# Optimization experiments

Measured on AMD Instinct MI355X. Metric: run time of the kernel, lower is better.

The kernel has to match this reference:

```python
import jax, jax.numpy as jnp
import numpy as np

B, C, H, W = 4, 384, 128, 128
HEADS = 8
EPS = 1e-12  # torch F.normalize default eps


def setup_inputs() -> dict:
    key = jax.random.key(0)
    k1, k2, k3, k4 = jax.random.split(key, 4)
    in1 = jax.random.normal(k1, (B, C, H, W), dtype=jnp.float32)
    in2 = jax.random.normal(k2, (B, C, H, W), dtype=jnp.float32)
    temperature = jnp.ones((HEADS, 1, 1), dtype=jnp.float32)
    proj_w = jax.random.normal(k3, (C, C), dtype=jnp.float32) * (1.0 / np.sqrt(C))
    proj_b = jax.random.normal(k4, (C,), dtype=jnp.float32) * 0.01
    return {"in1": in1, "in2": in2, "temperature": temperature,
            "proj_w": proj_w, "proj_b": proj_b}


def _l2norm_last(x):
    # torch F.normalize(dim=-1): x / max(||x||_2, eps)
    n = jnp.sqrt(jnp.sum(x * x, axis=-1, keepdims=True))
    return x / jnp.maximum(n, EPS)


def reference(in1, in2, temperature, proj_w, proj_b):
    b, c, h, w = in1.shape
    hd = c // HEADS  # per-head channels
    # b (head c) h w -> b head c (h w)
    q = in1.reshape(b, HEADS, hd, h * w)
    k = in2.reshape(b, HEADS, hd, h * w)
    q = _l2norm_last(q)
    k = _l2norm_last(k)
    # channel attention: [b, head, hd, hd]
    attn = jnp.einsum('bhcn,bhdn->bhcd', q, k) * temperature[None]
    attn = jax.nn.softmax(attn, axis=-1)
    out = jnp.einsum('bhcd,bhdn->bhcn', attn, k)  # [b, head, hd, HW]
    out = out.reshape(b, c, h, w)
    # 1x1 conv projection
    out = jnp.einsum('oc,bchw->bohw', proj_w, out) + proj_b[None, :, None, None]
    return out
```

## Files before the change

kernel.cpp:

```cpp
#include <hip/hip_runtime.h>
#include <hip/hip_bf16.h>

#define NB 4
#define CC 384
#define HEADS 8
#define HD 48
#define NN 16384
#define NROWS (NB*CC)

typedef __attribute__((ext_vector_type(8))) short bf16x8;
typedef __attribute__((ext_vector_type(4))) float f32x4;

__device__ __forceinline__ unsigned short f2bf(float f) {
  __hip_bfloat16 h = __float2bfloat16(f);
  return __builtin_bit_cast(unsigned short, h);
}
__device__ __forceinline__ unsigned int packbf(float a, float b) {
  return (unsigned int)f2bf(a) | ((unsigned int)f2bf(b) << 16);
}
__device__ __forceinline__ float bf2f(short s) {
  unsigned int u = ((unsigned int)(unsigned short)s) << 16;
  return __builtin_bit_cast(float, u);
}

__global__ __launch_bounds__(256) void k_copy(
    const float* __restrict__ in1, const float* __restrict__ in2,
    unsigned short* __restrict__ qbf, unsigned short* __restrict__ kbf)
{
  const float4* src = (const float4*)(blockIdx.y ? in2 : in1);
  uint4* dst = (uint4*)(blockIdx.y ? kbf : qbf);
  const int n = NROWS * NN / 8;
  int stride = gridDim.x * 256;
  for (int i = blockIdx.x * 256 + threadIdx.x; i < n; i += stride) {
    float4 v0 = src[2*i], v1 = src[2*i+1];
    uint4 o;
    o.x = packbf(v0.x, v0.y); o.y = packbf(v0.z, v0.w);
    o.z = packbf(v1.x, v1.y); o.w = packbf(v1.z, v1.w);
    dst[i] = o;
  }
}

__global__ __launch_bounds__(256) void k_gram(
    const unsigned short* __restrict__ qbf, const unsigned short* __restrict__ kbf,
    float* __restrict__ partial, float* __restrict__ sumsq_part)
{
  int bh = blockIdx.x;
  int chunk = blockIdx.y;
  int wave = threadIdx.x >> 6, lane = threadIdx.x & 63;
  int b = bh >> 3, h = bh & 7;
  size_t base = ((size_t)(b*CC + h*HD)) * NN;
  int lrow = lane & 15, lk = (lane >> 4) << 3;
  int kstart = chunk*1024 + wave*256;
  f32x4 acc[3][3] = {};
  float sq[3] = {0.f,0.f,0.f}, sk[3] = {0.f,0.f,0.f};
  for (int ks = 0; ks < 8; ++ks) {
    int kpos = kstart + ks*32 + lk;
    bf16x8 a[3], bb[3];
    #pragma unroll
    for (int t = 0; t < 3; ++t) {
      int rr = t*16 + lrow;
      a[t]  = *(const bf16x8*)(qbf + base + (size_t)rr * NN + kpos);
      bb[t] = *(const bf16x8*)(kbf + base + (size_t)rr * NN + kpos);
    }
    #pragma unroll
    for (int t = 0; t < 3; ++t) {
      #pragma unroll
      for (int j = 0; j < 8; ++j) {
        float fa = bf2f(a[t][j]);  sq[t] += fa*fa;
        float fb = bf2f(bb[t][j]); sk[t] += fb*fb;
      }
    }
    #pragma unroll
    for (int i = 0; i < 3; ++i)
      #pragma unroll
      for (int j = 0; j < 3; ++j)
        acc[i][j] = __builtin_amdgcn_mfma_f32_16x16x32_bf16(a[i], bb[j], acc[i][j], 0, 0, 0);
  }
  __shared__ float red[4][HD][HD+1];
  __shared__ float sqs[4][96];
  #pragma unroll
  for (int t = 0; t < 3; ++t) {
    float s = sq[t]; s += __shfl_xor(s, 16); s += __shfl_xor(s, 32);
    if (lane < 16) sqs[wave][t*16 + lane] = s;
    float s2 = sk[t]; s2 += __shfl_xor(s2, 16); s2 += __shfl_xor(s2, 32);
    if (lane < 16) sqs[wave][48 + t*16 + lane] = s2;
  }
  #pragma unroll
  for (int i = 0; i < 3; ++i)
    #pragma unroll
    for (int j = 0; j < 3; ++j)
      #pragma unroll
      for (int m = 0; m < 4; ++m) {
        int rr = i*16 + (lane>>4)*4 + m;
        int cc2 = j*16 + (lane&15);
        red[wave][rr][cc2] = acc[i][j][m];
      }
  __syncthreads();
  float* pout = partial + ((size_t)bh*16 + chunk) * (HD*HD);
  for (int e = threadIdx.x; e < HD*HD; e += 256) {
    int r = e / HD, c = e % HD;
    pout[e] = red[0][r][c] + red[1][r][c] + red[2][r][c] + red[3][r][c];
  }
  if (threadIdx.x < 96) {
    float* sout = sumsq_part + ((size_t)bh*16 + chunk) * 96;
    sout[threadIdx.x] = sqs[0][threadIdx.x] + sqs[1][threadIdx.x]
                      + sqs[2][threadIdx.x] + sqs[3][threadIdx.x];
  }
}

__global__ __launch_bounds__(256) void k_redsm(
    const float* __restrict__ partial, const float* __restrict__ sumsq_part,
    const float* __restrict__ temp, float* __restrict__ attn_out,
    float* __restrict__ rinv_k_g)
{
  int bh = blockIdx.x; int b = bh >> 3, h = bh & 7;
  __shared__ float attn[HD][HD+1];
  __shared__ float rqs[HD], rks[HD];
  if (threadIdx.x < 96) {
    float s = 0.f;
    #pragma unroll
    for (int c = 0; c < 16; ++c)
      s += sumsq_part[((size_t)bh*16 + c)*96 + threadIdx.x];
    float rinv = 1.f / fmaxf(sqrtf(s), 1e-12f);
    if (threadIdx.x < 48) rqs[threadIdx.x] = rinv;
    else { rks[threadIdx.x-48] = rinv; rinv_k_g[b*CC + h*HD + threadIdx.x-48] = rinv; }
  }
  const float* p = partial + (size_t)bh * 16 * (HD*HD);
  float tscale = temp[h];
  __syncthreads();
  for (int e = threadIdx.x; e < HD*HD; e += 256) {
    float s = 0.f;
    #pragma unroll
    for (int c2 = 0; c2 < 16; ++c2) s += p[c2*(HD*HD) + e];
    attn[e/HD][e%HD] = s * tscale * rqs[e/HD] * rks[e%HD];
  }
  __syncthreads();
  if (threadIdx.x < HD) {
    float* rowp = attn[threadIdx.x];
    float m = rowp[0];
    for (int j = 1; j < HD; ++j) m = fmaxf(m, rowp[j]);
    float sum = 0.f;
    for (int j = 0; j < HD; ++j) { float e = expf(rowp[j]-m); rowp[j] = e; sum += e; }
    float inv = 1.f / sum;
    for (int j = 0; j < HD; ++j) rowp[j] *= inv;
  }
  __syncthreads();
  float* ao = attn_out + (size_t)bh * (HD*HD);
  for (int e = threadIdx.x; e < HD*HD; e += 256)
    ao[e] = attn[e/HD][e%HD];
}

__global__ __launch_bounds__(256) void k_m(
    const float* __restrict__ attn, const float* __restrict__ proj_w,
    const float* __restrict__ rinv_k, unsigned short* __restrict__ Mbf)
{
  int b = blockIdx.x, ot = blockIdx.y;
  int o0 = ot * 16;
  __shared__ float sw[16*CC];
  __shared__ float sa[HEADS*HD*HD];
  const float* ab = attn + (size_t)b * HEADS * HD * HD;
  for (int i = threadIdx.x; i < HEADS*HD*HD; i += 256) sa[i] = ab[i];
  for (int i = threadIdx.x; i < 16*CC; i += 256)
    sw[i] = proj_w[(size_t)(o0 + i/CC)*CC + (i%CC)];
  __syncthreads();
  for (int idx = threadIdx.x; idx < 16*96; idx += 256) {
    int o = idx / 96, c4 = idx % 96;
    int col = c4 * 4;
    int h = col / HD, d = col % HD;
    const float* wp = sw + o*CC + h*HD;
    const float* ap = sa + h*HD*HD + d;
    f32x4 s = {0.f, 0.f, 0.f, 0.f};
    #pragma unroll
    for (int c2 = 0; c2 < HD; ++c2) {
      float w = wp[c2];
      f32x4 av = *(const f32x4*)(ap + c2*HD);
      s += w * av;
    }
    f32x4 rk = *(const f32x4*)(rinv_k + b*CC + col);
    s *= rk;
    ushort4 o4;
    o4.x = f2bf(s[0]); o4.y = f2bf(s[1]); o4.z = f2bf(s[2]); o4.w = f2bf(s[3]);
    *(ushort4*)(Mbf + ((size_t)b*CC + o0 + o)*CC + col) = o4;
  }
}

#define BM 128
#define BN 128
#define BK 64

__global__ __launch_bounds__(256) void k_final(
    const unsigned short* __restrict__ kbf, const unsigned short* __restrict__ Mbf,
    const float* __restrict__ bias, float* __restrict__ out)
{
  int b = blockIdx.z;
  int bm = blockIdx.y * BM, bn = blockIdx.x * BN;
  int tid = threadIdx.x, lane = tid & 63, wave = tid >> 6;
  int wrow = wave >> 1, wcol = wave & 1;
  __shared__ unsigned short Bt[BN * BK];
  char* btb = (char*)Bt;
  const unsigned short* kb = kbf + (size_t)b * CC * NN;
  const unsigned short* Mb = Mbf + (size_t)b * CC * CC;
  f32x4 acc[4][4] = {};
  int lrow = lane & 15, lkg = lane >> 4;
  for (int k0 = 0; k0 < CC; k0 += BK) {
    #pragma unroll
    for (int s = 0; s < 2; ++s) {
      int slot = tid + s*256;
      int cp = slot >> 4;
      int ng = slot & 15;
      int n0 = ng * 8;
      int c = k0 + cp*2;
      union { uint4 q; unsigned short u[8]; } r0, r1;
      r0.q = *(const uint4*)(kb + (size_t)c*NN + bn + n0);
      r1.q = *(const uint4*)(kb + (size_t)(c+1)*NN + bn + n0);
      #pragma unroll
      for (int i = 0; i < 8; ++i) {
        int n = n0 + i;
        unsigned int val = (unsigned int)r0.u[i] | ((unsigned int)r1.u[i] << 16);
        int pc = (cp>>2) ^ (n & 7) ^ ((n >> 3) & 7);
        *(unsigned int*)(btb + n*128 + (pc<<4) + ((cp&3)<<2)) = val;
      }
    }
    __syncthreads();
    #pragma unroll
    for (int kk = 0; kk < BK; kk += 32) {
      bf16x8 af[4], bfr[4];
      #pragma unroll
      for (int t = 0; t < 4; ++t) {
        int o = bm + wrow*64 + t*16 + lrow;
        af[t] = *(const bf16x8*)(Mb + (size_t)o*CC + (k0 + kk + (lkg<<3)));
        int n = wcol*64 + t*16 + lrow;
        int lc = (kk>>3) + lkg;
        int pc = lc ^ (n & 7) ^ ((n >> 3) & 7);
        bfr[t] = *(const bf16x8*)(btb + n*128 + (pc<<4));
      }
      #pragma unroll
      for (int i = 0; i < 4; ++i)
        #pragma unroll
        for (int j = 0; j < 4; ++j)
          acc[i][j] = __builtin_amdgcn_mfma_f32_16x16x32_bf16(af[i], bfr[j], acc[i][j], 0, 0, 0);
    }
    __syncthreads();
  }
  #pragma unroll
  for (int i = 0; i < 4; ++i) {
    int obase = bm + wrow*64 + i*16 + lkg*4;
    #pragma unroll
    for (int j = 0; j < 4; ++j) {
      int n = bn + wcol*64 + j*16 + lrow;
      #pragma unroll
      for (int m = 0; m < 4; ++m) {
        int o = obase + m;
        out[((size_t)b*CC + o)*NN + n] = acc[i][j][m] + bias[o];
      }
    }
  }
}

extern "C" void kernel_launch(void* const* d_in, const int* in_sizes, int n_in,
                              void* d_out, int out_size, void* d_ws, size_t ws_size,
                              hipStream_t stream)
{
  const float* in1    = (const float*)d_in[0];
  const float* in2    = (const float*)d_in[1];
  const float* temp   = (const float*)d_in[2];
  const float* proj_w = (const float*)d_in[3];
  const float* proj_b = (const float*)d_in[4];
  float* out = (float*)d_out;
  char* ws = (char*)d_ws;

  size_t off = 0;
  unsigned short* qbf = (unsigned short*)(ws + off); off += (size_t)NROWS*NN*2;
  unsigned short* kbf = (unsigned short*)(ws + off); off += (size_t)NROWS*NN*2;
  float* partial    = (float*)(ws + off); off += (size_t)32*16*HD*HD*4;
  float* sumsq_part = (float*)(ws + off); off += (size_t)32*16*96*4;
  float* attn_out   = (float*)(ws + off); off += (size_t)32*HD*HD*4;
  float* rinv_k     = (float*)(ws + off); off += NROWS*4;
  unsigned short* Mbf = (unsigned short*)(ws + off);

  k_copy<<<dim3(1024, 2), dim3(256), 0, stream>>>(in1, in2, qbf, kbf);
  k_gram<<<dim3(32, 16), dim3(256), 0, stream>>>(qbf, kbf, partial, sumsq_part);
  k_redsm<<<dim3(32), dim3(256), 0, stream>>>(partial, sumsq_part, temp, attn_out, rinv_k);
  k_m<<<dim3(NB, 24), dim3(256), 0, stream>>>(attn_out, proj_w, rinv_k, Mbf);
  k_final<<<dim3(NN/BN, CC/BM, NB), dim3(256), 0, stream>>>(kbf, Mbf, proj_b, out);
}
```

Before: 160.1 us.

## Fuse fp32-to-bf16 conversion into gram and final GEMM, drop copy kernel

Removes the standalone conversion kernel that wrote bf16 copies of both inputs. The gram kernel and the final projection GEMM now read the fp32 inputs directly and convert to bf16 in registers. The gram grid doubles its chunk count to keep parallelism, and sum-of-squares is now taken on fp32 values. This cuts a full write-then-read pass over the intermediate buffers, at the cost of the final GEMM loading twice the bytes per element of K.

```diff
diff --git a/kernel.cpp b/kernel.cpp
--- a/kernel.cpp
+++ b/kernel.cpp
@@ -18,30 +18,9 @@
 __device__ __forceinline__ unsigned int packbf(float a, float b) {
   return (unsigned int)f2bf(a) | ((unsigned int)f2bf(b) << 16);
 }
-__device__ __forceinline__ float bf2f(short s) {
-  unsigned int u = ((unsigned int)(unsigned short)s) << 16;
-  return __builtin_bit_cast(float, u);
-}
-
-__global__ __launch_bounds__(256) void k_copy(
+
+__global__ __launch_bounds__(256) void k_gram(
     const float* __restrict__ in1, const float* __restrict__ in2,
-    unsigned short* __restrict__ qbf, unsigned short* __restrict__ kbf)
-{
-  const float4* src = (const float4*)(blockIdx.y ? in2 : in1);
-  uint4* dst = (uint4*)(blockIdx.y ? kbf : qbf);
-  const int n = NROWS * NN / 8;
-  int stride = gridDim.x * 256;
-  for (int i = blockIdx.x * 256 + threadIdx.x; i < n; i += stride) {
-    float4 v0 = src[2*i], v1 = src[2*i+1];
-    uint4 o;
-    o.x = packbf(v0.x, v0.y); o.y = packbf(v0.z, v0.w);
-    o.z = packbf(v1.x, v1.y); o.w = packbf(v1.z, v1.w);
-    dst[i] = o;
-  }
-}
-
-__global__ __launch_bounds__(256) void k_gram(
-    const unsigned short* __restrict__ qbf, const unsigned short* __restrict__ kbf,
     float* __restrict__ partial, float* __restrict__ sumsq_part)
 {
   int bh = blockIdx.x;
@@ -50,25 +29,29 @@
   int b = bh >> 3, h = bh & 7;
   size_t base = ((size_t)(b*CC + h*HD)) * NN;
   int lrow = lane & 15, lk = (lane >> 4) << 3;
-  int kstart = chunk*1024 + wave*256;
+  int kstart = chunk*512 + wave*128;
   f32x4 acc[3][3] = {};
   float sq[3] = {0.f,0.f,0.f}, sk[3] = {0.f,0.f,0.f};
-  for (int ks = 0; ks < 8; ++ks) {
+  for (int ks = 0; ks < 4; ++ks) {
     int kpos = kstart + ks*32 + lk;
     bf16x8 a[3], bb[3];
     #pragma unroll
     for (int t = 0; t < 3; ++t) {
       int rr = t*16 + lrow;
-      a[t]  = *(const bf16x8*)(qbf + base + (size_t)rr * NN + kpos);
-      bb[t] = *(const bf16x8*)(kbf + base + (size_t)rr * NN + kpos);
-    }
-    #pragma unroll
-    for (int t = 0; t < 3; ++t) {
-      #pragma unroll
-      for (int j = 0; j < 8; ++j) {
-        float fa = bf2f(a[t][j]);  sq[t] += fa*fa;
-        float fb = bf2f(bb[t][j]); sk[t] += fb*fb;
-      }
+      const float* pq = in1 + base + (size_t)rr * NN + kpos;
+      const float* pk = in2 + base + (size_t)rr * NN + kpos;
+      float4 q0 = *(const float4*)pq, q1 = *((const float4*)pq + 1);
+      float4 k0 = *(const float4*)pk, k1 = *((const float4*)pk + 1);
+      union { bf16x8 v; unsigned short u[8]; } ua, ub;
+      ua.u[0]=f2bf(q0.x); ua.u[1]=f2bf(q0.y); ua.u[2]=f2bf(q0.z); ua.u[3]=f2bf(q0.w);
+      ua.u[4]=f2bf(q1.x); ua.u[5]=f2bf(q1.y); ua.u[6]=f2bf(q1.z); ua.u[7]=f2bf(q1.w);
+      ub.u[0]=f2bf(k0.x); ub.u[1]=f2bf(k0.y); ub.u[2]=f2bf(k0.z); ub.u[3]=f2bf(k0.w);
+      ub.u[4]=f2bf(k1.x); ub.u[5]=f2bf(k1.y); ub.u[6]=f2bf(k1.z); ub.u[7]=f2bf(k1.w);
+      a[t] = ua.v; bb[t] = ub.v;
+      sq[t] += q0.x*q0.x + q0.y*q0.y + q0.z*q0.z + q0.w*q0.w
+             + q1.x*q1.x + q1.y*q1.y + q1.z*q1.z + q1.w*q1.w;
+      sk[t] += k0.x*k0.x + k0.y*k0.y + k0.z*k0.z + k0.w*k0.w
+             + k1.x*k1.x + k1.y*k1.y + k1.z*k1.z + k1.w*k1.w;
     }
     #pragma unroll
     for (int i = 0; i < 3; ++i)
@@ -96,13 +79,13 @@
         red[wave][rr][cc2] = acc[i][j][m];
       }
   __syncthreads();
-  float* pout = partial + ((size_t)bh*16 + chunk) * (HD*HD);
+  float* pout = partial + ((size_t)bh*32 + chunk) * (HD*HD);
   for (int e = threadIdx.x; e < HD*HD; e += 256) {
     int r = e / HD, c = e % HD;
     pout[e] = red[0][r][c] + red[1][r][c] + red[2][r][c] + red[3][r][c];
   }
   if (threadIdx.x < 96) {
-    float* sout = sumsq_part + ((size_t)bh*16 + chunk) * 96;
+    float* sout = sumsq_part + ((size_t)bh*32 + chunk) * 96;
     sout[threadIdx.x] = sqs[0][threadIdx.x] + sqs[1][threadIdx.x]
                       + sqs[2][threadIdx.x] + sqs[3][threadIdx.x];
   }
@@ -119,19 +102,19 @@
   if (threadIdx.x < 96) {
     float s = 0.f;
     #pragma unroll
-    for (int c = 0; c < 16; ++c)
-      s += sumsq_part[((size_t)bh*16 + c)*96 + threadIdx.x];
+    for (int c = 0; c < 32; ++c)
+      s += sumsq_part[((size_t)bh*32 + c)*96 + threadIdx.x];
     float rinv = 1.f / fmaxf(sqrtf(s), 1e-12f);
     if (threadIdx.x < 48) rqs[threadIdx.x] = rinv;
     else { rks[threadIdx.x-48] = rinv; rinv_k_g[b*CC + h*HD + threadIdx.x-48] = rinv; }
   }
-  const float* p = partial + (size_t)bh * 16 * (HD*HD);
+  const float* p = partial + (size_t)bh * 32 * (HD*HD);
   float tscale = temp[h];
   __syncthreads();
   for (int e = threadIdx.x; e < HD*HD; e += 256) {
     float s = 0.f;
     #pragma unroll
-    for (int c2 = 0; c2 < 16; ++c2) s += p[c2*(HD*HD) + e];
+    for (int c2 = 0; c2 < 32; ++c2) s += p[c2*(HD*HD) + e];
     attn[e/HD][e%HD] = s * tscale * rqs[e/HD] * rks[e%HD];
   }
   __syncthreads();
@@ -189,7 +172,7 @@
 #define BK 64
 
 __global__ __launch_bounds__(256) void k_final(
-    const unsigned short* __restrict__ kbf, const unsigned short* __restrict__ Mbf,
+    const float* __restrict__ in2, const unsigned short* __restrict__ Mbf,
     const float* __restrict__ bias, float* __restrict__ out)
 {
   int b = blockIdx.z;
@@ -198,7 +181,7 @@
   int wrow = wave >> 1, wcol = wave & 1;
   __shared__ unsigned short Bt[BN * BK];
   char* btb = (char*)Bt;
-  const unsigned short* kb = kbf + (size_t)b * CC * NN;
+  const float* kb = in2 + (size_t)b * CC * NN;
   const unsigned short* Mb = Mbf + (size_t)b * CC * CC;
   f32x4 acc[4][4] = {};
   int lrow = lane & 15, lkg = lane >> 4;
@@ -210,13 +193,16 @@
       int ng = slot & 15;
       int n0 = ng * 8;
       int c = k0 + cp*2;
-      union { uint4 q; unsigned short u[8]; } r0, r1;
-      r0.q = *(const uint4*)(kb + (size_t)c*NN + bn + n0);
-      r1.q = *(const uint4*)(kb + (size_t)(c+1)*NN + bn + n0);
+      const float* p0 = kb + (size_t)c*NN + bn + n0;
+      const float* p1 = kb + (size_t)(c+1)*NN + bn + n0;
+      float4 a0 = *(const float4*)p0, a1 = *((const float4*)p0 + 1);
+      float4 b0 = *(const float4*)p1, b1 = *((const float4*)p1 + 1);
+      float lo[8] = {a0.x,a0.y,a0.z,a0.w,a1.x,a1.y,a1.z,a1.w};
+      float hi[8] = {b0.x,b0.y,b0.z,b0.w,b1.x,b1.y,b1.z,b1.w};
       #pragma unroll
       for (int i = 0; i < 8; ++i) {
         int n = n0 + i;
-        unsigned int val = (unsigned int)r0.u[i] | ((unsigned int)r1.u[i] << 16);
+        unsigned int val = packbf(lo[i], hi[i]);
         int pc = (cp>>2) ^ (n & 7) ^ ((n >> 3) & 7);
         *(unsigned int*)(btb + n*128 + (pc<<4) + ((cp&3)<<2)) = val;
       }
@@ -270,17 +256,14 @@
   char* ws = (char*)d_ws;
 
   size_t off = 0;
-  unsigned short* qbf = (unsigned short*)(ws + off); off += (size_t)NROWS*NN*2;
-  unsigned short* kbf = (unsigned short*)(ws + off); off += (size_t)NROWS*NN*2;
-  float* partial    = (float*)(ws + off); off += (size_t)32*16*HD*HD*4;
-  float* sumsq_part = (float*)(ws + off); off += (size_t)32*16*96*4;
+  float* partial    = (float*)(ws + off); off += (size_t)32*32*HD*HD*4;
+  float* sumsq_part = (float*)(ws + off); off += (size_t)32*32*96*4;
   float* attn_out   = (float*)(ws + off); off += (size_t)32*HD*HD*4;
   float* rinv_k     = (float*)(ws + off); off += NROWS*4;
   unsigned short* Mbf = (unsigned short*)(ws + off);
 
-  k_copy<<<dim3(1024, 2), dim3(256), 0, stream>>>(in1, in2, qbf, kbf);
-  k_gram<<<dim3(32, 16), dim3(256), 0, stream>>>(qbf, kbf, partial, sumsq_part);
+  k_gram<<<dim3(32, 32), dim3(256), 0, stream>>>(in1, in2, partial, sumsq_part);
   k_redsm<<<dim3(32), dim3(256), 0, stream>>>(partial, sumsq_part, temp, attn_out, rinv_k);
   k_m<<<dim3(NB, 24), dim3(256), 0, stream>>>(attn_out, proj_w, rinv_k, Mbf);
-  k_final<<<dim3(NN/BN, CC/BM, NB), dim3(256), 0, stream>>>(kbf, Mbf, proj_b, out);
-}
+  k_final<<<dim3(NN/BN, CC/BM, NB), dim3(256), 0, stream>>>(in2, Mbf, proj_b, out);
+}
```

Result: faster. 142.8 us (-10.8%).
